# Performance work log

Measured on AMD Instinct MI355X. Metric: run time of the kernel, lower is better.

## Reference

```python
import jax, jax.numpy as jnp
import numpy as np

H, W = 14, 14
HEAD_DIM = 32
HEADS = 24
HIDDEN = 768
RATE = 0.2
EPS = 1e-5


def _bias_idxs(h, w):
    # map_bias indexing: for flat pair index x over (h*w)^2
    x = jnp.arange(h * h * w * w)
    m, n = x // (h * w), x % (h * w)
    i, j = m // w, m % w
    ip, jp = n // w, n % w
    return (i - ip + h) * (2 * w) + (j - jp + w)


def _layer_norm(x, g, b):
    mu = jnp.mean(x, axis=-1, keepdims=True)
    var = jnp.mean(jnp.square(x - mu), axis=-1, keepdims=True)
    return (x - mu) * jax.lax.rsqrt(var + EPS) * g + b


def setup_inputs() -> dict:
    key = jax.random.key(0)
    ks = jax.random.split(key, 10)
    N, L = 64, H * W
    s = lambda fan_in: 1.0 / np.sqrt(fan_in)
    return {
        "x": jax.random.normal(ks[0], (N, L, HIDDEN), jnp.float32),
        "rel_bias": jax.random.uniform(ks[1], (1, 2 * H * 2 * W), jnp.float32, -0.5, 0.5),
        "wq": jax.random.normal(ks[2], (HEAD_DIM, HEAD_DIM), jnp.float32) * s(HEAD_DIM),
        "wk": jax.random.normal(ks[3], (HEAD_DIM, HEAD_DIM), jnp.float32) * s(HEAD_DIM),
        "wv": jax.random.normal(ks[4], (HEAD_DIM, HEAD_DIM), jnp.float32) * s(HEAD_DIM),
        "w_out": jax.random.normal(ks[5], (HIDDEN, HIDDEN), jnp.float32) * s(HIDDEN),
        "ln1_g": jnp.ones((HIDDEN,), jnp.float32),
        "ln1_b": jnp.zeros((HIDDEN,), jnp.float32),
        "ln2_g": jnp.ones((HIDDEN,), jnp.float32),
        "ln2_b": jnp.zeros((HIDDEN,), jnp.float32),
        "w1": jax.random.normal(ks[6], (4 * HIDDEN, HIDDEN), jnp.float32) * s(HIDDEN),
        "b1": jnp.zeros((4 * HIDDEN,), jnp.float32),
        "w2": jax.random.normal(ks[7], (HIDDEN, 4 * HIDDEN), jnp.float32) * s(4 * HIDDEN),
        "b2": jnp.zeros((HIDDEN,), jnp.float32),
    }


def reference(x, rel_bias, wq, wk, wv, w_out, ln1_g, ln1_b, ln2_g, ln2_b, w1, b1, w2, b2):
    N, L, _ = x.shape

    def attn(m):
        xh = m.reshape(N, L, HEADS, HEAD_DIM)
        # Linear(head_dim, head_dim) shared across heads; torch Linear: y = x @ W^T
        q = jnp.einsum("nlhd,ed->nlhe", xh, wq)
        k = jnp.einsum("nlhd,ed->nlhe", xh, wk)
        v = jnp.einsum("nlhd,ed->nlhe", xh, wv)
        scores = jnp.einsum("nqhd,nkhd->nhqk", q, k)
        bias = rel_bias[0][_bias_idxs(H, W)].reshape(1, 1, L, L)
        a = jax.nn.softmax((scores + bias) / np.sqrt(HEAD_DIM), axis=-1)
        o = jnp.einsum("nhqk,nkhd->nqhd", a, v).reshape(N, L, HIDDEN)
        return o @ w_out.T

    def ffn(m):
        h = jax.nn.gelu(m @ w1.T + b1, approximate=False)
        return h @ w2.T + b2

    # training-mode stochastic depth: deterministic scaling by RATE
    x = (x + attn(_layer_norm(x, ln1_g, ln1_b))) * RATE
    x = (x + ffn(_layer_norm(x, ln2_g, ln2_b))) * RATE
    return x
```

## Files before the change

### kernel.cpp

```cpp
#include <hip/hip_runtime.h>
#include <math.h>

#define NB    64
#define LSEQ  196
#define HID   768
#define NHEAD 24
#define HDIM  32
#define FFN   3072
#define ROWS  (NB * LSEQ)
#define RATE  0.2f
#define LN_EPS 1e-5f

typedef unsigned short bf16_t;
typedef short s16x8 __attribute__((ext_vector_type(8)));
typedef float f32x4 __attribute__((ext_vector_type(4)));

__device__ __forceinline__ unsigned short f2bf(float f) {
    unsigned u = __float_as_uint(f);
    unsigned r = u + 0x7fffu + ((u >> 16) & 1u);
    return (unsigned short)(r >> 16);
}

#define GLOAD_LDS16(g, l)                                                  \
    __builtin_amdgcn_global_load_lds(                                      \
        (const __attribute__((address_space(1))) void*)(g),                \
        (__attribute__((address_space(3))) void*)(l), 16, 0, 0)

#define WOUT4 (HID * HID / 4)
#define W14   (FFN * HID / 4)
__global__ __launch_bounds__(256) void cvt_w_kernel(
    const float* __restrict__ w_out, const float* __restrict__ w1,
    const float* __restrict__ w2, bf16_t* __restrict__ wob,
    bf16_t* __restrict__ w1b, bf16_t* __restrict__ w2b)
{
    int i = blockIdx.x * 256 + threadIdx.x;
    const float* src; bf16_t* dst; int off;
    if (i < WOUT4)            { src = w_out; dst = wob; off = i; }
    else if (i < WOUT4 + W14) { src = w1;    dst = w1b; off = i - WOUT4; }
    else                      { src = w2;    dst = w2b; off = i - WOUT4 - W14; }
    float4 v = ((const float4*)src)[off];
    uint2 p;
    p.x = (unsigned)f2bf(v.x) | ((unsigned)f2bf(v.y) << 16);
    p.y = (unsigned)f2bf(v.z) | ((unsigned)f2bf(v.w) << 16);
    ((uint2*)dst)[off] = p;
}

__global__ __launch_bounds__(256) void ln_kernel(
    const float* __restrict__ x, const float* __restrict__ g,
    const float* __restrict__ b, bf16_t* __restrict__ yv)
{
    int row = blockIdx.x;
    int tid = threadIdx.x;
    const float* xr = x + (size_t)row * HID;
    float v0 = xr[tid], v1 = xr[tid + 256], v2 = xr[tid + 512];
    __shared__ float rs[256], rs2[256];
    rs[tid]  = v0 + v1 + v2;
    rs2[tid] = v0 * v0 + v1 * v1 + v2 * v2;
    __syncthreads();
    for (int off = 128; off > 0; off >>= 1) {
        if (tid < off) { rs[tid] += rs[tid + off]; rs2[tid] += rs2[tid + off]; }
        __syncthreads();
    }
    float mean = rs[0] * (1.0f / HID);
    float var  = rs2[0] * (1.0f / HID) - mean * mean;
    float rstd = rsqrtf(var + LN_EPS);
    bf16_t* yr = yv + (size_t)row * HID;
    yr[tid]       = f2bf((v0 - mean) * rstd * g[tid]       + b[tid]);
    yr[tid + 256] = f2bf((v1 - mean) * rstd * g[tid + 256] + b[tid + 256]);
    yr[tid + 512] = f2bf((v2 - mean) * rstd * g[tid + 512] + b[tid + 512]);
}

#define QKV_T 16
__global__ __launch_bounds__(256) void ln_qkv_mfma_kernel(
    const float* __restrict__ x, const float* __restrict__ g,
    const float* __restrict__ b,
    const float* __restrict__ wq, const float* __restrict__ wk,
    const float* __restrict__ wv,
    bf16_t* __restrict__ q, bf16_t* __restrict__ k, bf16_t* __restrict__ v)
{
    int tid = threadIdx.x;
    int w = tid >> 6, lane = tid & 63;
    int lr = lane & 15, lq = lane >> 4;

    __shared__ __align__(16) bf16_t Xs[QKV_T * 24 * 32];
    __shared__ __align__(16) bf16_t Wqs[32 * 32];
    __shared__ __align__(16) bf16_t Wks[32 * 32];
    __shared__ __align__(16) bf16_t Wvs[32 * 32];

    for (int i = tid; i < 1024; i += 256) {
        Wqs[i] = f2bf(wq[i]);
        Wks[i] = f2bf(wk[i]);
        Wvs[i] = f2bf(wv[i]);
    }

    float4 gv[3], bv[3];
#pragma unroll
    for (int i = 0; i < 3; i++) {
        gv[i] = ((const float4*)g)[lane + i * 64];
        bv[i] = ((const float4*)b)[lane + i * 64];
    }

    for (int j = 0; j < 4; j++) {
        int lt = w * 4 + j;
        size_t row = (size_t)blockIdx.x * QKV_T + lt;
        const float4* xr = (const float4*)(x + row * HID);
        float4 xv[3];
        float s = 0.f, s2 = 0.f;
#pragma unroll
        for (int i = 0; i < 3; i++) {
            xv[i] = xr[lane + i * 64];
            s  += xv[i].x + xv[i].y + xv[i].z + xv[i].w;
            s2 += xv[i].x * xv[i].x + xv[i].y * xv[i].y
                + xv[i].z * xv[i].z + xv[i].w * xv[i].w;
        }
#pragma unroll
        for (int d = 1; d < 64; d <<= 1) {
            s  += __shfl_xor(s, d);
            s2 += __shfl_xor(s2, d);
        }
        float mean = s * (1.0f / HID);
        float rstd = rsqrtf(s2 * (1.0f / HID) - mean * mean + LN_EPS);
#pragma unroll
        for (int i = 0; i < 3; i++) {
            int idx  = (lane + i * 64) * 4;
            int head = idx >> 5, d0 = idx & 31;
            float o0 = (xv[i].x - mean) * rstd * gv[i].x + bv[i].x;
            float o1 = (xv[i].y - mean) * rstd * gv[i].y + bv[i].y;
            float o2 = (xv[i].z - mean) * rstd * gv[i].z + bv[i].z;
            float o3 = (xv[i].w - mean) * rstd * gv[i].w + bv[i].w;
            uint2 p;
            p.x = (unsigned)f2bf(o0) | ((unsigned)f2bf(o1) << 16);
            p.y = (unsigned)f2bf(o2) | ((unsigned)f2bf(o3) << 16);
            *(uint2*)&Xs[(lt * 24 + head) * 32 + d0] = p;
        }
    }
    __syncthreads();

    s16x8 bq[2], bk[2], bvv[2];
    bq[0]  = *(const s16x8*)&Wqs[lr * 32 + lq * 8];
    bq[1]  = *(const s16x8*)&Wqs[(16 + lr) * 32 + lq * 8];
    bk[0]  = *(const s16x8*)&Wks[lr * 32 + lq * 8];
    bk[1]  = *(const s16x8*)&Wks[(16 + lr) * 32 + lq * 8];
    bvv[0] = *(const s16x8*)&Wvs[lr * 32 + lq * 8];
    bvv[1] = *(const s16x8*)&Wvs[(16 + lr) * 32 + lq * 8];

    for (int t = 0; t < 6; t++) {
        int tile = w * 6 + t;
        s16x8 aX = *(const s16x8*)&Xs[(tile * 16 + lr) * 32 + lq * 8];
        f32x4 z = {};
        f32x4 aq0 = __builtin_amdgcn_mfma_f32_16x16x32_bf16(aX, bq[0],  z, 0, 0, 0);
        f32x4 aq1 = __builtin_amdgcn_mfma_f32_16x16x32_bf16(aX, bq[1],  z, 0, 0, 0);
        f32x4 ak0 = __builtin_amdgcn_mfma_f32_16x16x32_bf16(aX, bk[0],  z, 0, 0, 0);
        f32x4 ak1 = __builtin_amdgcn_mfma_f32_16x16x32_bf16(aX, bk[1],  z, 0, 0, 0);
        f32x4 av0 = __builtin_amdgcn_mfma_f32_16x16x32_bf16(aX, bvv[0], z, 0, 0, 0);
        f32x4 av1 = __builtin_amdgcn_mfma_f32_16x16x32_bf16(aX, bvv[1], z, 0, 0, 0);
        int rbase = tile * 16 + lq * 4;
#pragma unroll
        for (int r = 0; r < 4; r++) {
            int xrow = rbase + r;
            int t_loc = xrow / 24, head = xrow - t_loc * 24;
            size_t gb = ((size_t)blockIdx.x * QKV_T + t_loc) * HID + head * 32;
            q[gb + lr]      = f2bf(aq0[r]);
            q[gb + 16 + lr] = f2bf(aq1[r]);
            k[gb + lr]      = f2bf(ak0[r]);
            k[gb + 16 + lr] = f2bf(ak1[r]);
            v[gb + lr]      = f2bf(av0[r]);
            v[gb + 16 + lr] = f2bf(av1[r]);
        }
    }
}

#define VT_S 232
#define P_S  40

__global__ __launch_bounds__(256) void attn_mfma_kernel(
    const bf16_t* __restrict__ q, const bf16_t* __restrict__ k,
    const bf16_t* __restrict__ v, const float* __restrict__ rel_bias,
    bf16_t* __restrict__ o)
{
    int h = blockIdx.x;
    int n = blockIdx.y;
    int tid = threadIdx.x;
    int w = tid >> 6, lane = tid & 63;
    int lr = lane & 15;
    int lq = lane >> 4;

    __shared__ __align__(16) bf16_t Qs[208 * 32];
    __shared__ __align__(16) bf16_t Ks[224 * 32];
    __shared__ __align__(16) bf16_t Vt[32 * VT_S];
    __shared__ float bsh[28 * 28];
    __shared__ __align__(16) bf16_t Ps[4][16 * P_S];

    size_t base = (size_t)n * LSEQ * HID + (size_t)h * HDIM;

    for (int i = tid; i < 224 * 4; i += 256) {
        int r = i >> 2, c = i & 3;
        uint4 kv = make_uint4(0, 0, 0, 0);
        if (r < 196) kv = *(const uint4*)&k[base + (size_t)r * HID + c * 8];
        *(uint4*)&Ks[r * 32 + c * 8] = kv;
        if (r < 208) {
            uint4 qv = make_uint4(0, 0, 0, 0);
            if (r < 196) qv = *(const uint4*)&q[base + (size_t)r * HID + c * 8];
            *(uint4*)&Qs[r * 32 + c * 8] = qv;
        }
    }
    for (int i = tid; i < 196 * 16; i += 256) {
        int key = i >> 4, d2 = (i & 15) * 2;
        unsigned u = *(const unsigned*)&v[base + (size_t)key * HID + d2];
        Vt[d2 * VT_S + key]       = (bf16_t)(u & 0xffffu);
        Vt[(d2 + 1) * VT_S + key] = (bf16_t)(u >> 16);
    }
    for (int i = tid; i < 32 * 32; i += 256) {
        int d = i >> 5, kp = i & 31;
        if (kp < 28) Vt[d * VT_S + 196 + kp] = 0;
    }
    for (int i = tid; i < 784; i += 256) bsh[i] = rel_bias[i];
    __syncthreads();

    const float inv_sqrt_d = 0.17677669529663687f;
    bf16_t* P = Ps[w];

    for (int qt = w; qt < 13; qt += 4) {
        s16x8 aQ = *(const s16x8*)&Qs[(qt * 16 + lr) * 32 + lq * 8];

        int bb[4]; bool qvalid[4];
#pragma unroll
        for (int r = 0; r < 4; r++) {
            int qr = qt * 16 + lq * 4 + r;
            qvalid[r] = qr < LSEQ;
            int qq = qvalid[r] ? qr : 0;
            int qi = qq / 14, qj = qq - 14 * (qq / 14);
            bb[r] = (qi + 14) * 28 + (qj + 14);
        }

        f32x4 sf[14];
#pragma unroll
        for (int kt = 0; kt < 14; kt++) {
            s16x8 bK = *(const s16x8*)&Ks[(kt * 16 + lr) * 32 + lq * 8];
            f32x4 z = {};
            sf[kt] = __builtin_amdgcn_mfma_f32_16x16x32_bf16(aQ, bK, z, 0, 0, 0);
        }
#pragma unroll
        for (int kt = 0; kt < 14; kt++) {
            int key = kt * 16 + lr;
            bool kv = key < LSEQ;
            int kk2 = kv ? key : 0;
            int ip = kk2 / 14, jp = kk2 - 14 * ip;
            int boff = ip * 28 + jp;
#pragma unroll
            for (int r = 0; r < 4; r++) {
                float val = (sf[kt][r] + bsh[bb[r] - boff]) * inv_sqrt_d;
                sf[kt][r] = kv ? val : -1e30f;
            }
        }
        float mx[4];
#pragma unroll
        for (int r = 0; r < 4; r++) {
            float m = sf[0][r];
#pragma unroll
            for (int kt = 1; kt < 14; kt++) m = fmaxf(m, sf[kt][r]);
            mx[r] = m;
        }
#pragma unroll
        for (int d = 1; d < 16; d <<= 1)
#pragma unroll
            for (int r = 0; r < 4; r++)
                mx[r] = fmaxf(mx[r], __shfl_xor(mx[r], d));
        float sum[4] = {0.f, 0.f, 0.f, 0.f};
#pragma unroll
        for (int kt = 0; kt < 14; kt++)
#pragma unroll
            for (int r = 0; r < 4; r++) {
                float p = __expf(sf[kt][r] - mx[r]);
                sf[kt][r] = p;
                sum[r] += p;
            }
#pragma unroll
        for (int d = 1; d < 16; d <<= 1)
#pragma unroll
            for (int r = 0; r < 4; r++)
                sum[r] += __shfl_xor(sum[r], d);

        f32x4 oacc[2] = {};
#pragma unroll
        for (int kc = 0; kc < 7; kc++) {
#pragma unroll
            for (int r = 0; r < 4; r++) {
                P[(lq * 4 + r) * P_S + lr]      = f2bf(sf[2 * kc][r]);
                P[(lq * 4 + r) * P_S + 16 + lr] = f2bf(sf[2 * kc + 1][r]);
            }
            s16x8 aP = *(const s16x8*)&P[lr * P_S + lq * 8];
#pragma unroll
            for (int dt = 0; dt < 2; dt++) {
                s16x8 bV = *(const s16x8*)&Vt[(dt * 16 + lr) * VT_S + kc * 32 + lq * 8];
                oacc[dt] = __builtin_amdgcn_mfma_f32_16x16x32_bf16(aP, bV, oacc[dt], 0, 0, 0);
            }
        }
#pragma unroll
        for (int r = 0; r < 4; r++) {
            if (qvalid[r]) {
                float inv_l = 1.0f / sum[r];
                size_t ob = base + (size_t)(qt * 16 + lq * 4 + r) * HID;
                o[ob + lr]      = f2bf(oacc[0][r] * inv_l);
                o[ob + 16 + lr] = f2bf(oacc[1][r] * inv_l);
            }
        }
    }
}

__device__ __forceinline__ float gelu_fast(float x) {
    float z2 = 1.5957691216f * (x + 0.044715f * x * x * x);
    return x - x * __frcp_rn(__expf(z2) + 1.0f);
}

template <int MODE, bool OBF, int TM>
__global__ __launch_bounds__(256) void gemm_mfma(
    const bf16_t* __restrict__ A, const bf16_t* __restrict__ B,
    void* __restrict__ Cv, int M, int N, int K,
    const float* __restrict__ bias, const float* __restrict__ res, float scale)
{
    constexpr int MT = TM / 32;
    __shared__ __align__(16) bf16_t As[2][TM * 64];
    __shared__ __align__(16) bf16_t Bs[2][128 * 64];

    int tid = threadIdx.x;
    int mb = M / TM, nb = N >> 7;
    int gblk = blockIdx.x;
    int full = mb & ~7;
    int gfull = full * nb;
    int m_, n_;
    if (gblk < gfull) {
        int sg = gblk / (8 * nb), u = gblk - sg * (8 * nb);
        m_ = sg * 8 + (u & 7); n_ = u >> 3;
    } else {
        int u = gblk - gfull, rem = mb - full;
        m_ = full + u % rem; n_ = u / rem;
    }
    int bm = m_ * TM, bn = n_ << 7;

    int w    = tid >> 6;
    int lane = tid & 63;
    int wm = (w & 1) * (TM / 2);
    int wn = (w >> 1) * 64;
    int lr = lane & 15;
    int lq = lane >> 4;

    int srowl = lane >> 3;
    int scb   = ((lane & 7) ^ srowl) * 16;
    const char* Ab = (const char*)A;
    const char* Bb = (const char*)B;

    f32x4 acc[MT][4] = {};

    auto stage = [&](int k0, int bi) {
#pragma unroll
        for (int j = 0; j < TM / 32; j++) {
            int rb = w * (TM / 4) + j * 8;
            GLOAD_LDS16(Ab + ((size_t)(bm + rb + srowl) * K + k0) * 2 + scb,
                        &As[bi][rb * 64]);
        }
#pragma unroll
        for (int j = 0; j < 4; j++) {
            int rb = w * 32 + j * 8;
            GLOAD_LDS16(Bb + ((size_t)(bn + rb + srowl) * K + k0) * 2 + scb,
                        &Bs[bi][rb * 64]);
        }
    };

    auto compute = [&](int bi) {
        int sw = lr & 7;
#pragma unroll
        for (int kc = 0; kc < 2; kc++) {
            int cof = (((kc << 2) | lq) ^ sw) * 8;
            s16x8 af[MT], bf[4];
#pragma unroll
            for (int t = 0; t < MT; t++)
                af[t] = *(const s16x8*)&As[bi][(wm + t * 16 + lr) * 64 + cof];
#pragma unroll
            for (int t = 0; t < 4; t++)
                bf[t] = *(const s16x8*)&Bs[bi][(wn + t * 16 + lr) * 64 + cof];
#pragma unroll
            for (int tm = 0; tm < MT; tm++)
#pragma unroll
                for (int tn = 0; tn < 4; tn++)
                    acc[tm][tn] = __builtin_amdgcn_mfma_f32_16x16x32_bf16(
                        af[tm], bf[tn], acc[tm][tn], 0, 0, 0);
        }
    };

    stage(0, 0);
    asm volatile("s_waitcnt vmcnt(0)" ::: "memory");
    __builtin_amdgcn_s_barrier();

    const int nt = K >> 6;
    int cur = 0;
    for (int t = 0; t < nt - 1; ++t) {
        stage((t + 1) << 6, cur ^ 1);
        compute(cur);
        asm volatile("s_waitcnt vmcnt(0)" ::: "memory");
        __builtin_amdgcn_s_barrier();
        cur ^= 1;
    }
    compute(cur);

#pragma unroll
    for (int tm = 0; tm < MT; tm++) {
#pragma unroll
        for (int tn = 0; tn < 4; tn++) {
#pragma unroll
            for (int r = 0; r < 4; r++) {
                int mrow = bm + wm + tm * 16 + lq * 4 + r;
                int ncol = bn + wn + tn * 16 + lr;
                float vacc = acc[tm][tn][r];
                if (MODE == 1) {
                    vacc = (res[(size_t)mrow * N + ncol] + vacc) * scale;
                } else if (MODE == 2) {
                    vacc = gelu_fast(vacc + bias[ncol]);
                } else if (MODE == 3) {
                    vacc = (res[(size_t)mrow * N + ncol] + vacc + bias[ncol]) * scale;
                }
                if (OBF) ((bf16_t*)Cv)[(size_t)mrow * N + ncol] = f2bf(vacc);
                else     ((float*)Cv)[(size_t)mrow * N + ncol] = vacc;
            }
        }
    }
}

template <int MODE, bool OBF>
__global__ __launch_bounds__(512, 2) void gemm_fph(
    const bf16_t* __restrict__ A, const bf16_t* __restrict__ B,
    void* __restrict__ Cv, int M, int N, int K,
    const float* __restrict__ bias, const float* __restrict__ res, float scale)
{
    constexpr int BM = 256, BN = 128, BK = 64, NBUF = 3;
    __shared__ __align__(16) bf16_t As[NBUF][BM * BK];
    __shared__ __align__(16) bf16_t Bs[NBUF][BN * BK];

    int tid  = threadIdx.x;
    int w    = tid >> 6;
    int lane = tid & 63;

    int mb = M / BM, nb = N / BN;
    int gblk = blockIdx.x;
    int full = mb & ~7;
    int gfull = full * nb;
    int m_, n_;
    if (gblk < gfull) {
        int sg = gblk / (8 * nb), u = gblk - sg * (8 * nb);
        m_ = sg * 8 + (u & 7); n_ = u >> 3;
    } else {
        int u = gblk - gfull, rem = mb - full;
        m_ = full + u % rem; n_ = u / rem;
    }
    int bm = m_ * BM, bn = n_ * BN;

    int wm = (w >> 1) * 64;
    int wn = (w & 1) * 64;
    int lr = lane & 15;
    int lq = lane >> 4;

    int srowl = lane >> 3;
    int scb   = ((lane & 7) ^ srowl) * 16;
    const char* Ab = (const char*)A;
    const char* Bb = (const char*)B;

    f32x4 acc[4][4] = {};

    auto stageA = [&](int t, int bi, int j) {
        int rb = j * 64 + w * 8;
        GLOAD_LDS16(Ab + ((size_t)(bm + rb + srowl) * K + t * BK) * 2 + scb,
                    &As[bi][rb * BK]);
    };
    auto stageB = [&](int t, int bi, int j) {
        int rb = j * 64 + w * 8;
        GLOAD_LDS16(Bb + ((size_t)(bn + rb + srowl) * K + t * BK) * 2 + scb,
                    &Bs[bi][rb * BK]);
    };

    const int NT = K / BK;
    int sw = lr & 7;

    stageA(0, 0, 0); stageA(0, 0, 1); stageA(0, 0, 2); stageA(0, 0, 3);
    stageB(0, 0, 0); stageB(0, 0, 1);
    stageA(1, 1, 0); stageA(1, 1, 1); stageA(1, 1, 2); stageA(1, 1, 3);
    stageB(1, 1, 0); stageB(1, 1, 1);
    asm volatile("s_waitcnt vmcnt(6)" ::: "memory");
    __builtin_amdgcn_s_barrier();

    for (int t = 0; t < NT; ++t) {
        int ct = t % 3;
        bool st = (t + 2) < NT;
        int bs2 = (t + 2) % 3;
        const bf16_t* Ac = As[ct];
        const bf16_t* Bc = Bs[ct];

        {
            int cof = ((lq) ^ sw) * 8;
            s16x8 af[4], bf4[4];
#pragma unroll
            for (int i = 0; i < 4; i++)
                af[i] = *(const s16x8*)&Ac[(wm + i * 16 + lr) * BK + cof];
#pragma unroll
            for (int i = 0; i < 4; i++)
                bf4[i] = *(const s16x8*)&Bc[(wn + i * 16 + lr) * BK + cof];
            if (st) { stageA(t + 2, bs2, 0); stageA(t + 2, bs2, 1); stageA(t + 2, bs2, 2); }
            __builtin_amdgcn_s_barrier();
            __builtin_amdgcn_s_setprio(1);
#pragma unroll
            for (int tm = 0; tm < 4; tm++)
#pragma unroll
                for (int tn = 0; tn < 4; tn++)
                    acc[tm][tn] = __builtin_amdgcn_mfma_f32_16x16x32_bf16(
                        af[tm], bf4[tn], acc[tm][tn], 0, 0, 0);
            __builtin_amdgcn_s_setprio(0);
        }
        __builtin_amdgcn_s_barrier();

        {
            int cof = ((4 | lq) ^ sw) * 8;
            s16x8 af[4], bf4[4];
#pragma unroll
            for (int i = 0; i < 4; i++)
                af[i] = *(const s16x8*)&Ac[(wm + i * 16 + lr) * BK + cof];
#pragma unroll
            for (int i = 0; i < 4; i++)
                bf4[i] = *(const s16x8*)&Bc[(wn + i * 16 + lr) * BK + cof];
            if (st) { stageA(t + 2, bs2, 3); stageB(t + 2, bs2, 0); stageB(t + 2, bs2, 1); }
            __builtin_amdgcn_s_barrier();
            __builtin_amdgcn_s_setprio(1);
#pragma unroll
            for (int tm = 0; tm < 4; tm++)
#pragma unroll
                for (int tn = 0; tn < 4; tn++)
                    acc[tm][tn] = __builtin_amdgcn_mfma_f32_16x16x32_bf16(
                        af[tm], bf4[tn], acc[tm][tn], 0, 0, 0);
            __builtin_amdgcn_s_setprio(0);
        }

        if (t < NT - 1) {
            if (st) asm volatile("s_waitcnt vmcnt(6)" ::: "memory");
            else    asm volatile("s_waitcnt vmcnt(0)" ::: "memory");
            __builtin_amdgcn_s_barrier();
        }
    }

#pragma unroll
    for (int tm = 0; tm < 4; tm++) {
#pragma unroll
        for (int tn = 0; tn < 4; tn++) {
#pragma unroll
            for (int r = 0; r < 4; r++) {
                int mrow = bm + wm + tm * 16 + lq * 4 + r;
                int ncol = bn + wn + tn * 16 + lr;
                float vacc = acc[tm][tn][r];
                if (MODE == 1) {
                    vacc = (res[(size_t)mrow * N + ncol] + vacc) * scale;
                } else if (MODE == 2) {
                    vacc = gelu_fast(vacc + bias[ncol]);
                } else if (MODE == 3) {
                    vacc = (res[(size_t)mrow * N + ncol] + vacc + bias[ncol]) * scale;
                }
                if (OBF) ((bf16_t*)Cv)[(size_t)mrow * N + ncol] = f2bf(vacc);
                else     ((float*)Cv)[(size_t)mrow * N + ncol] = vacc;
            }
        }
    }
}

extern "C" void kernel_launch(void* const* d_in, const int* in_sizes, int n_in,
                              void* d_out, int out_size, void* d_ws, size_t ws_size,
                              hipStream_t stream)
{
    const float* x        = (const float*)d_in[0];
    const float* rel_bias = (const float*)d_in[1];
    const float* wq       = (const float*)d_in[2];
    const float* wk       = (const float*)d_in[3];
    const float* wv       = (const float*)d_in[4];
    const float* w_out    = (const float*)d_in[5];
    const float* ln1_g    = (const float*)d_in[6];
    const float* ln1_b    = (const float*)d_in[7];
    const float* ln2_g    = (const float*)d_in[8];
    const float* ln2_b    = (const float*)d_in[9];
    const float* w1       = (const float*)d_in[10];
    const float* b1       = (const float*)d_in[11];
    const float* w2       = (const float*)d_in[12];
    const float* b2       = (const float*)d_in[13];
    float* out = (float*)d_out;
    float* ws  = (float*)d_ws;

    const size_t SZ = (size_t)ROWS * HID;
    bf16_t* q_bf = (bf16_t*)(ws + SZ);
    bf16_t* k_bf = (bf16_t*)(ws + 2 * SZ);
    bf16_t* v_bf = (bf16_t*)(ws + 3 * SZ);
    bf16_t* o_bf = (bf16_t*)ws;
    bf16_t* y2b  = (bf16_t*)(ws + SZ / 2);
    bf16_t* h    = (bf16_t*)(ws + SZ);
    bf16_t* wob  = (bf16_t*)(ws + 4 * SZ);
    bf16_t* w1b  = wob + (size_t)HID * HID;
    bf16_t* w2b  = w1b + (size_t)FFN * HID;

    cvt_w_kernel<<<(WOUT4 + 2 * W14 + 255) / 256, 256, 0, stream>>>(
        w_out, w1, w2, wob, w1b, w2b);

    ln_qkv_mfma_kernel<<<ROWS / QKV_T, 256, 0, stream>>>(
        x, ln1_g, ln1_b, wq, wk, wv, q_bf, k_bf, v_bf);

    attn_mfma_kernel<<<dim3(NHEAD, NB), 256, 0, stream>>>(q_bf, k_bf, v_bf, rel_bias, o_bf);

    gemm_mfma<1, false, 64><<<(ROWS / 64) * (HID / 128), 256, 0, stream>>>(
        o_bf, wob, out, ROWS, HID, HID, nullptr, x, RATE);

    ln_kernel<<<ROWS, 256, 0, stream>>>(out, ln2_g, ln2_b, y2b);

    gemm_fph<2, true><<<(ROWS / 256) * (FFN / 128), 512, 0, stream>>>(
        y2b, w1b, h, ROWS, FFN, HID, b1, nullptr, 1.0f);

    gemm_mfma<3, false, 64><<<(ROWS / 64) * (HID / 128), 256, 0, stream>>>(
        h, w2b, out, ROWS, HID, FFN, b2, out, RATE);
}
```

Measured before the change: 433.8 us.

## Use triple-buffered pipelined GEMM for narrow N projections and drop mid-iteration barriers

Replaces the double-buffered 64x128 gemm_mfma used for the output projection and FFN down-projection with a new 3-stage pipelined kernel (gemm_pipe3), which prefetches two K-tiles ahead and splits the loads across the two half-K compute phases. Also removes the two intra-iteration barriers in the large FFN up-projection kernel and swaps the modulo buffer indexing for a rotating counter. The aim is to hide global-to-LDS latency and cut synchronisation stalls. Removing barriers risks a race if a wave refills a buffer another wave is still reading, and the extra LDS buffer may lower occupancy.

```diff
diff --git a/kernel.cpp b/kernel.cpp
--- a/kernel.cpp
+++ b/kernel.cpp
@@ -313,18 +313,21 @@
     return x - x * __frcp_rn(__expf(z2) + 1.0f);
 }
 
-template <int MODE, bool OBF, int TM>
-__global__ __launch_bounds__(256) void gemm_mfma(
+template <int MODE, bool OBF>
+__global__ __launch_bounds__(512, 2) void gemm_fph(
     const bf16_t* __restrict__ A, const bf16_t* __restrict__ B,
     void* __restrict__ Cv, int M, int N, int K,
     const float* __restrict__ bias, const float* __restrict__ res, float scale)
 {
-    constexpr int MT = TM / 32;
-    __shared__ __align__(16) bf16_t As[2][TM * 64];
-    __shared__ __align__(16) bf16_t Bs[2][128 * 64];
-
-    int tid = threadIdx.x;
-    int mb = M / TM, nb = N >> 7;
+    constexpr int BM = 256, BN = 128, BK = 64, NBUF = 3;
+    __shared__ __align__(16) bf16_t As[NBUF][BM * BK];
+    __shared__ __align__(16) bf16_t Bs[NBUF][BN * BK];
+
+    int tid  = threadIdx.x;
+    int w    = tid >> 6;
+    int lane = tid & 63;
+
+    int mb = M / BM, nb = N / BN;
     int gblk = blockIdx.x;
     int full = mb & ~7;
     int gfull = full * nb;
@@ -336,12 +339,10 @@
         int u = gblk - gfull, rem = mb - full;
         m_ = full + u % rem; n_ = u / rem;
     }
-    int bm = m_ * TM, bn = n_ << 7;
-
-    int w    = tid >> 6;
-    int lane = tid & 63;
-    int wm = (w & 1) * (TM / 2);
-    int wn = (w >> 1) * 64;
+    int bm = m_ * BM, bn = n_ * BN;
+
+    int wm = (w >> 1) * 64;
+    int wn = (w & 1) * 64;
     int lr = lane & 15;
     int lq = lane >> 4;
 
@@ -350,61 +351,85 @@
     const char* Ab = (const char*)A;
     const char* Bb = (const char*)B;
 
-    f32x4 acc[MT][4] = {};
-
-    auto stage = [&](int k0, int bi) {
-#pragma unroll
-        for (int j = 0; j < TM / 32; j++) {
-            int rb = w * (TM / 4) + j * 8;
-            GLOAD_LDS16(Ab + ((size_t)(bm + rb + srowl) * K + k0) * 2 + scb,
-                        &As[bi][rb * 64]);
-        }
-#pragma unroll
-        for (int j = 0; j < 4; j++) {
-            int rb = w * 32 + j * 8;
-            GLOAD_LDS16(Bb + ((size_t)(bn + rb + srowl) * K + k0) * 2 + scb,
-                        &Bs[bi][rb * 64]);
-        }
+    f32x4 acc[4][4] = {};
+
+    auto stageA = [&](int t, int bi, int j) {
+        int rb = j * 64 + w * 8;
+        GLOAD_LDS16(Ab + ((size_t)(bm + rb + srowl) * K + t * BK) * 2 + scb,
+                    &As[bi][rb * BK]);
     };
-
-    auto compute = [&](int bi) {
-        int sw = lr & 7;
-#pragma unroll
-        for (int kc = 0; kc < 2; kc++) {
-            int cof = (((kc << 2) | lq) ^ sw) * 8;
-            s16x8 af[MT], bf[4];
-#pragma unroll
-            for (int t = 0; t < MT; t++)
-                af[t] = *(const s16x8*)&As[bi][(wm + t * 16 + lr) * 64 + cof];
-#pragma unroll
-            for (int t = 0; t < 4; t++)
-                bf[t] = *(const s16x8*)&Bs[bi][(wn + t * 16 + lr) * 64 + cof];
-#pragma unroll
-            for (int tm = 0; tm < MT; tm++)
+    auto stageB = [&](int t, int bi, int j) {
+        int rb = j * 64 + w * 8;
+        GLOAD_LDS16(Bb + ((size_t)(bn + rb + srowl) * K + t * BK) * 2 + scb,
+                    &Bs[bi][rb * BK]);
+    };
+
+    const int NT = K / BK;
+    int sw = lr & 7;
+
+    stageA(0, 0, 0); stageA(0, 0, 1); stageA(0, 0, 2); stageA(0, 0, 3);
+    stageB(0, 0, 0); stageB(0, 0, 1);
+    stageA(1, 1, 0); stageA(1, 1, 1); stageA(1, 1, 2); stageA(1, 1, 3);
+    stageB(1, 1, 0); stageB(1, 1, 1);
+    asm volatile("s_waitcnt vmcnt(6)" ::: "memory");
+    __builtin_amdgcn_s_barrier();
+
+    int ct = 0;
+    for (int t = 0; t < NT; ++t) {
+        bool st = (t + 2) < NT;
+        int bs2 = (ct == 0) ? 2 : ct - 1;
+        const bf16_t* Ac = As[ct];
+        const bf16_t* Bc = Bs[ct];
+
+        {
+            int cof = (lq ^ sw) * 8;
+            s16x8 af[4], bf4[4];
+#pragma unroll
+            for (int i = 0; i < 4; i++)
+                af[i] = *(const s16x8*)&Ac[(wm + i * 16 + lr) * BK + cof];
+#pragma unroll
+            for (int i = 0; i < 4; i++)
+                bf4[i] = *(const s16x8*)&Bc[(wn + i * 16 + lr) * BK + cof];
+            if (st) { stageA(t + 2, bs2, 0); stageA(t + 2, bs2, 1); stageA(t + 2, bs2, 2); }
+            __builtin_amdgcn_s_setprio(1);
+#pragma unroll
+            for (int tm = 0; tm < 4; tm++)
 #pragma unroll
                 for (int tn = 0; tn < 4; tn++)
                     acc[tm][tn] = __builtin_amdgcn_mfma_f32_16x16x32_bf16(
-                        af[tm], bf[tn], acc[tm][tn], 0, 0, 0);
-        }
-    };
-
-    stage(0, 0);
-    asm volatile("s_waitcnt vmcnt(0)" ::: "memory");
-    __builtin_amdgcn_s_barrier();
-
-    const int nt = K >> 6;
-    int cur = 0;
-    for (int t = 0; t < nt - 1; ++t) {
-        stage((t + 1) << 6, cur ^ 1);
-        compute(cur);
-        asm volatile("s_waitcnt vmcnt(0)" ::: "memory");
-        __builtin_amdgcn_s_barrier();
-        cur ^= 1;
-    }
-    compute(cur);
-
-#pragma unroll
-    for (int tm = 0; tm < MT; tm++) {
+                        af[tm], bf4[tn], acc[tm][tn], 0, 0, 0);
+            __builtin_amdgcn_s_setprio(0);
+        }
+        {
+            int cof = ((4 | lq) ^ sw) * 8;
+            s16x8 af[4], bf4[4];
+#pragma unroll
+            for (int i = 0; i < 4; i++)
+                af[i] = *(const s16x8*)&Ac[(wm + i * 16 + lr) * BK + cof];
+#pragma unroll
+            for (int i = 0; i < 4; i++)
+                bf4[i] = *(const s16x8*)&Bc[(wn + i * 16 + lr) * BK + cof];
+            if (st) { stageA(t + 2, bs2, 3); stageB(t + 2, bs2, 0); stageB(t + 2, bs2, 1); }
+            __builtin_amdgcn_s_setprio(1);
+#pragma unroll
+            for (int tm = 0; tm < 4; tm++)
+#pragma unroll
+                for (int tn = 0; tn < 4; tn++)
+                    acc[tm][tn] = __builtin_amdgcn_mfma_f32_16x16x32_bf16(
+                        af[tm], bf4[tn], acc[tm][tn], 0, 0, 0);
+            __builtin_amdgcn_s_setprio(0);
+        }
+
+        if (t < NT - 1) {
+            if (st) asm volatile("s_waitcnt vmcnt(6)" ::: "memory");
+            else    asm volatile("s_waitcnt vmcnt(0)" ::: "memory");
+            __builtin_amdgcn_s_barrier();
+        }
+        ct = (ct == 2) ? 0 : ct + 1;
+    }
+
+#pragma unroll
+    for (int tm = 0; tm < 4; tm++) {
 #pragma unroll
         for (int tn = 0; tn < 4; tn++) {
 #pragma unroll
@@ -427,12 +452,12 @@
 }
 
 template <int MODE, bool OBF>
-__global__ __launch_bounds__(512, 2) void gemm_fph(
+__global__ __launch_bounds__(256) void gemm_pipe3(
     const bf16_t* __restrict__ A, const bf16_t* __restrict__ B,
     void* __restrict__ Cv, int M, int N, int K,
     const float* __restrict__ bias, const float* __restrict__ res, float scale)
 {
-    constexpr int BM = 256, BN = 128, BK = 64, NBUF = 3;
+    constexpr int BM = 64, BN = 128, BK = 64, NBUF = 3;
     __shared__ __align__(16) bf16_t As[NBUF][BM * BK];
     __shared__ __align__(16) bf16_t Bs[NBUF][BN * BK];
 
@@ -454,8 +479,8 @@
     }
     int bm = m_ * BM, bn = n_ * BN;
 
-    int wm = (w >> 1) * 64;
-    int wn = (w & 1) * 64;
+    int wm = (w & 1) * 32;
+    int wn = (w >> 1) * 64;
     int lr = lane & 15;
     int lq = lane >> 4;
 
@@ -464,15 +489,15 @@
     const char* Ab = (const char*)A;
     const char* Bb = (const char*)B;
 
-    f32x4 acc[4][4] = {};
+    f32x4 acc[2][4] = {};
 
     auto stageA = [&](int t, int bi, int j) {
-        int rb = j * 64 + w * 8;
+        int rb = j * 32 + w * 8;
         GLOAD_LDS16(Ab + ((size_t)(bm + rb + srowl) * K + t * BK) * 2 + scb,
                     &As[bi][rb * BK]);
     };
     auto stageB = [&](int t, int bi, int j) {
-        int rb = j * 64 + w * 8;
+        int rb = j * 32 + w * 8;
         GLOAD_LDS16(Bb + ((size_t)(bn + rb + srowl) * K + t * BK) * 2 + scb,
                     &Bs[bi][rb * BK]);
     };
@@ -480,56 +505,52 @@
     const int NT = K / BK;
     int sw = lr & 7;
 
-    stageA(0, 0, 0); stageA(0, 0, 1); stageA(0, 0, 2); stageA(0, 0, 3);
-    stageB(0, 0, 0); stageB(0, 0, 1);
-    stageA(1, 1, 0); stageA(1, 1, 1); stageA(1, 1, 2); stageA(1, 1, 3);
-    stageB(1, 1, 0); stageB(1, 1, 1);
+    stageA(0, 0, 0); stageA(0, 0, 1);
+    stageB(0, 0, 0); stageB(0, 0, 1); stageB(0, 0, 2); stageB(0, 0, 3);
+    stageA(1, 1, 0); stageA(1, 1, 1);
+    stageB(1, 1, 0); stageB(1, 1, 1); stageB(1, 1, 2); stageB(1, 1, 3);
     asm volatile("s_waitcnt vmcnt(6)" ::: "memory");
     __builtin_amdgcn_s_barrier();
 
+    int ct = 0;
     for (int t = 0; t < NT; ++t) {
-        int ct = t % 3;
         bool st = (t + 2) < NT;
-        int bs2 = (t + 2) % 3;
+        int bs2 = (ct == 0) ? 2 : ct - 1;
         const bf16_t* Ac = As[ct];
         const bf16_t* Bc = Bs[ct];
 
         {
-            int cof = ((lq) ^ sw) * 8;
-            s16x8 af[4], bf4[4];
-#pragma unroll
-            for (int i = 0; i < 4; i++)
+            int cof = (lq ^ sw) * 8;
+            s16x8 af[2], bf4[4];
+#pragma unroll
+            for (int i = 0; i < 2; i++)
                 af[i] = *(const s16x8*)&Ac[(wm + i * 16 + lr) * BK + cof];
 #pragma unroll
             for (int i = 0; i < 4; i++)
                 bf4[i] = *(const s16x8*)&Bc[(wn + i * 16 + lr) * BK + cof];
-            if (st) { stageA(t + 2, bs2, 0); stageA(t + 2, bs2, 1); stageA(t + 2, bs2, 2); }
-            __builtin_amdgcn_s_barrier();
+            if (st) { stageA(t + 2, bs2, 0); stageA(t + 2, bs2, 1); stageB(t + 2, bs2, 0); }
             __builtin_amdgcn_s_setprio(1);
 #pragma unroll
-            for (int tm = 0; tm < 4; tm++)
+            for (int tm = 0; tm < 2; tm++)
 #pragma unroll
                 for (int tn = 0; tn < 4; tn++)
                     acc[tm][tn] = __builtin_amdgcn_mfma_f32_16x16x32_bf16(
                         af[tm], bf4[tn], acc[tm][tn], 0, 0, 0);
             __builtin_amdgcn_s_setprio(0);
         }
-        __builtin_amdgcn_s_barrier();
-
         {
             int cof = ((4 | lq) ^ sw) * 8;
-            s16x8 af[4], bf4[4];
-#pragma unroll
-            for (int i = 0; i < 4; i++)
+            s16x8 af[2], bf4[4];
+#pragma unroll
+            for (int i = 0; i < 2; i++)
                 af[i] = *(const s16x8*)&Ac[(wm + i * 16 + lr) * BK + cof];
 #pragma unroll
             for (int i = 0; i < 4; i++)
                 bf4[i] = *(const s16x8*)&Bc[(wn + i * 16 + lr) * BK + cof];
-            if (st) { stageA(t + 2, bs2, 3); stageB(t + 2, bs2, 0); stageB(t + 2, bs2, 1); }
-            __builtin_amdgcn_s_barrier();
+            if (st) { stageB(t + 2, bs2, 1); stageB(t + 2, bs2, 2); stageB(t + 2, bs2, 3); }
             __builtin_amdgcn_s_setprio(1);
 #pragma unroll
-            for (int tm = 0; tm < 4; tm++)
+            for (int tm = 0; tm < 2; tm++)
 #pragma unroll
                 for (int tn = 0; tn < 4; tn++)
                     acc[tm][tn] = __builtin_amdgcn_mfma_f32_16x16x32_bf16(
@@ -542,10 +563,11 @@
             else    asm volatile("s_waitcnt vmcnt(0)" ::: "memory");
             __builtin_amdgcn_s_barrier();
         }
-    }
-
-#pragma unroll
-    for (int tm = 0; tm < 4; tm++) {
+        ct = (ct == 2) ? 0 : ct + 1;
+    }
+
+#pragma unroll
+    for (int tm = 0; tm < 2; tm++) {
 #pragma unroll
         for (int tn = 0; tn < 4; tn++) {
 #pragma unroll
@@ -607,7 +629,7 @@
 
     attn_mfma_kernel<<<dim3(NHEAD, NB), 256, 0, stream>>>(q_bf, k_bf, v_bf, rel_bias, o_bf);
 
-    gemm_mfma<1, false, 64><<<(ROWS / 64) * (HID / 128), 256, 0, stream>>>(
+    gemm_pipe3<1, false><<<(ROWS / 64) * (HID / 128), 256, 0, stream>>>(
         o_bf, wob, out, ROWS, HID, HID, nullptr, x, RATE);
 
     ln_kernel<<<ROWS, 256, 0, stream>>>(out, ln2_g, ln2_b, y2b);
@@ -615,6 +637,6 @@
     gemm_fph<2, true><<<(ROWS / 256) * (FFN / 128), 512, 0, stream>>>(
         y2b, w1b, h, ROWS, FFN, HID, b1, nullptr, 1.0f);
 
-    gemm_mfma<3, false, 64><<<(ROWS / 64) * (HID / 128), 256, 0, stream>>>(
+    gemm_pipe3<3, false><<<(ROWS / 64) * (HID / 128), 256, 0, stream>>>(
         h, w2b, out, ROWS, HID, FFN, b2, out, RATE);
 }
```

Measured after the change: 473.3 us. 1.09x slower.
